# Optimization experiments

Measured on AMD Instinct MI355X. Metric: run time of the kernel, lower is better.

The kernel has to match this reference:

```python
import jax, jax.numpy as jnp
import numpy as np

B, H, W = 4, 496, 496
M = 8  # max vertices of a quad-quad convex intersection


def _corners(boxes):
    # boxes [..., 7] = (x, y, z, dx, dy, dz, heading) -> CCW BEV corners [..., 4, 2]
    x, y, dx, dy, r = boxes[..., 0], boxes[..., 1], boxes[..., 3], boxes[..., 4], boxes[..., 6]
    lx = jnp.array([0.5, -0.5, -0.5, 0.5], dtype=boxes.dtype) * dx[..., None]
    ly = jnp.array([0.5, 0.5, -0.5, -0.5], dtype=boxes.dtype) * dy[..., None]
    c, s = jnp.cos(r)[..., None], jnp.sin(r)[..., None]
    cx = x[..., None] + c * lx - s * ly
    cy = y[..., None] + s * lx + c * ly
    return jnp.stack([cx, cy], axis=-1)


def _clip(poly, cnt, a, b):
    # Clip padded CCW polygon (poly [M,2], cnt valid verts) by halfplane left of edge a->b.
    idx = jnp.arange(M)
    valid = idx < cnt
    nidx = jnp.where(idx + 1 >= cnt, 0, idx + 1)
    cur, nxt = poly, poly[nidx]
    ex, ey = b[0] - a[0], b[1] - a[1]
    dc = ex * (cur[:, 1] - a[1]) - ey * (cur[:, 0] - a[0])  # signed dist of cur
    dn = ex * (nxt[:, 1] - a[1]) - ey * (nxt[:, 0] - a[0])
    inc, inn = dc >= 0, dn >= 0
    keep = inc & valid                      # emit cur if inside
    crs = (inc != inn) & valid              # emit edge/line intersection if crossing
    den = dc - dn
    t = dc / jnp.where(jnp.abs(den) < 1e-9, 1.0, den)
    ip = cur + t[:, None] * (nxt - cur)
    c = keep.astype(jnp.int32) + crs.astype(jnp.int32)
    offs = jnp.cumsum(c) - c                # exclusive prefix sum -> output slots
    out = jnp.zeros_like(poly)
    out = out.at[jnp.where(keep, offs, M)].set(cur, mode='drop')
    out = out.at[jnp.where(crs, offs + keep.astype(jnp.int32), M)].set(ip, mode='drop')
    return out, jnp.sum(c)


def _inter_area(ca, cb):
    # Intersection area of two CCW quads (each [4,2]) via Sutherland-Hodgman.
    poly = jnp.zeros((M, 2), ca.dtype).at[:4].set(ca)
    cnt = jnp.int32(4)
    for i in range(4):
        poly, cnt = _clip(poly, cnt, cb[i], cb[(i + 1) % 4])
    idx = jnp.arange(M)
    valid = idx < cnt
    nidx = jnp.where(idx + 1 >= cnt, 0, idx + 1)
    nxt = poly[nidx]
    cr = poly[:, 0] * nxt[:, 1] - nxt[:, 0] * poly[:, 1]  # shoelace terms
    return 0.5 * jnp.abs(jnp.sum(jnp.where(valid, cr, 0.0)))


def _iou3d_aligned(boxes_a, boxes_b):
    # Element-wise (aligned) 3D oriented-box IoU. boxes [N,7] -> iou [N].
    inter_bev = jax.vmap(_inter_area)(_corners(boxes_a), _corners(boxes_b))
    za0, za1 = boxes_a[:, 2] - 0.5 * boxes_a[:, 5], boxes_a[:, 2] + 0.5 * boxes_a[:, 5]
    zb0, zb1 = boxes_b[:, 2] - 0.5 * boxes_b[:, 5], boxes_b[:, 2] + 0.5 * boxes_b[:, 5]
    zo = jnp.maximum(jnp.minimum(za1, zb1) - jnp.maximum(za0, zb0), 0.0)
    inter_vol = inter_bev * zo
    vol_a = boxes_a[:, 3] * boxes_a[:, 4] * boxes_a[:, 5]
    vol_b = boxes_b[:, 3] * boxes_b[:, 4] * boxes_b[:, 5]
    return inter_vol / (vol_a + vol_b - inter_vol + 1e-7)


def setup_inputs() -> dict:
    key = jax.random.key(0)
    kc, kd, kr, kn, km, kp, ki = jax.random.split(key, 7)
    center = jax.random.normal(kc, (B, H, W, 3), dtype=jnp.float32) * 2.0
    dims = jax.random.uniform(kd, (B, H, W, 3), minval=0.5, maxval=3.0, dtype=jnp.float32)
    heading = jax.random.uniform(kr, (B, H, W, 1), minval=-np.pi, maxval=np.pi, dtype=jnp.float32)
    box_gt = jnp.concatenate([center, dims, heading], axis=-1)  # [B,H,W,7]
    pred = box_gt + jax.random.normal(kn, box_gt.shape, dtype=jnp.float32) * 0.1
    pred = pred.at[..., 3:6].set(jnp.maximum(pred[..., 3:6], 0.2))  # keep dims positive
    box_pred = jnp.transpose(pred, (0, 3, 1, 2))  # [B,7,H,W]
    mask = jax.random.randint(km, (B, H, W), 0, 2, dtype=jnp.int32)
    iou_pred = jax.random.normal(kp, (B, H, W), dtype=jnp.float32) * 0.5
    ind = jax.random.randint(ki, (B, 128), 0, H * W, dtype=jnp.int32)  # unused by the layer
    return {"iou_pred": iou_pred, "mask": mask, "ind": ind, "box_pred": box_pred, "box_gt": box_gt}


def reference(iou_pred, mask, ind, box_pred, box_gt):
    pred = jnp.transpose(box_pred, (0, 2, 3, 1)).reshape(-1, 7)  # [N,7]
    gt = box_gt.reshape(-1, 7)
    target = 2.0 * _iou3d_aligned(pred, gt) - 1.0               # [N]
    m = mask.astype(jnp.float32).reshape(-1)
    loss = jnp.sum(m * jnp.abs(iou_pred.reshape(-1) - target))
    return loss / (jnp.sum(m) + 1e-4)
```

## Files before the change

### kernel.cpp

```cpp
#include <hip/hip_runtime.h>
#include <math.h>

#define B_   4
#define H_   496
#define W_   496
#define HW_  (H_ * W_)
#define N_   (B_ * HW_)
#define NBLK (N_ / 256)

static_assert(N_ % 256 == 0, "no tail");

__device__ __forceinline__ float clip_sum(const float px[4], const float py[4],
                                          const float qx[4], const float qy[4]) {
    float ex[4], ey[4];
#pragma unroll
    for (int i = 0; i < 4; ++i) {
        ex[i] = qx[(i + 1) & 3] - qx[i];
        ey[i] = qy[(i + 1) & 3] - qy[i];
    }
    float F[4][4];
#pragma unroll
    for (int i = 0; i < 4; ++i)
#pragma unroll
        for (int k = 0; k < 4; ++k)
            F[i][k] = ex[i] * (py[k] - qy[i]) - ey[i] * (px[k] - qx[i]);

    float s = 0.f;
#pragma unroll
    for (int k = 0; k < 4; ++k) {
        const int   k1 = (k + 1) & 3;
        const float ax = px[k], ay = py[k];
        const float dx = px[k1] - ax, dy = py[k1] - ay;
        float t0 = 0.f, t1 = 1.f;
#pragma unroll
        for (int i = 0; i < 4; ++i) {
            const float fa = F[i][k], fb = F[i][k1];
            const float df = fb - fa;
            const float dfs = (df == 0.f) ? 1e-30f : df;
            const float tc = __fdividef(-fa, dfs);
            t0 = fmaxf(t0, (df > 0.f) ? tc : 0.f);
            t1 = fminf(t1, (df < 0.f) ? tc : 1.f);
            if (df == 0.f && fa < 0.f) t0 = 2.f;
        }
        const float x0 = ax + t0 * dx, y0 = ay + t0 * dy;
        const float x1 = ax + t1 * dx, y1 = ay + t1 * dy;
        const float c  = x0 * y1 - x1 * y0;
        s += (t1 > t0) ? c : 0.f;
    }
    return s;
}

__global__ __launch_bounds__(256) void iou_main(
    const float* __restrict__ iou_pred,
    const int*   __restrict__ mask,
    const float* __restrict__ box_pred,
    const float* __restrict__ box_gt,
    float* __restrict__ ws)
{
    __shared__ float rn[4], rd[4];
    const int tid = threadIdx.x;
    const int n = blockIdx.x * 256 + tid;

    const int b  = n / HW_;
    const int hw = n - b * HW_;

    const float* bp = box_pred + (size_t)b * 7 * HW_ + hw;
    const float pax = bp[0];
    const float pay = bp[1 * HW_];
    const float paz = bp[2 * HW_];
    const float pdx = bp[3 * HW_];
    const float pdy = bp[4 * HW_];
    const float pdz = bp[5 * HW_];
    const float pr  = bp[6 * HW_];

    const float* bg = box_gt + (size_t)n * 7;
    const float gax = bg[0], gay = bg[1], gaz = bg[2];
    const float gdx = bg[3], gdy = bg[4], gdz = bg[5], gr = bg[6];

    float sp, cp; __sincosf(pr, &sp, &cp);
    float sg, cg; __sincosf(gr, &sg, &cg);
    const float phx = 0.5f * pdx, phy = 0.5f * pdy;
    const float ghx = 0.5f * gdx, ghy = 0.5f * gdy;

    float px[4], py[4], qx[4], qy[4];
    px[0] = pax + cp * phx - sp * phy;  py[0] = pay + sp * phx + cp * phy;
    px[1] = pax - cp * phx - sp * phy;  py[1] = pay - sp * phx + cp * phy;
    px[2] = pax - cp * phx + sp * phy;  py[2] = pay - sp * phx - cp * phy;
    px[3] = pax + cp * phx + sp * phy;  py[3] = pay + sp * phx - cp * phy;
    qx[0] = gax + cg * ghx - sg * ghy;  qy[0] = gay + sg * ghx + cg * ghy;
    qx[1] = gax - cg * ghx - sg * ghy;  qy[1] = gay - sg * ghx + cg * ghy;
    qx[2] = gax - cg * ghx + sg * ghy;  qy[2] = gay - sg * ghx - cg * ghy;
    qx[3] = gax + cg * ghx + sg * ghy;  qy[3] = gay + sg * ghx - cg * ghy;

    const float inter_bev = 0.5f * (clip_sum(px, py, qx, qy) +
                                    clip_sum(qx, qy, px, py));

    const float za0 = paz - 0.5f * pdz, za1 = paz + 0.5f * pdz;
    const float zb0 = gaz - 0.5f * gdz, zb1 = gaz + 0.5f * gdz;
    const float zo  = fmaxf(fminf(za1, zb1) - fmaxf(za0, zb0), 0.f);
    const float iv  = inter_bev * zo;
    const float va  = pdx * pdy * pdz;
    const float vb  = gdx * gdy * gdz;
    const float iou = iv / (va + vb - iv + 1e-7f);
    const float target = 2.f * iou - 1.f;

    const float m = (float)mask[n];
    float num = m * fabsf(iou_pred[n] - target);
    float den = m;

#pragma unroll
    for (int off = 32; off > 0; off >>= 1) {
        num += __shfl_down(num, off);
        den += __shfl_down(den, off);
    }
    if ((tid & 63) == 0) { rn[tid >> 6] = num; rd[tid >> 6] = den; }
    __syncthreads();
    if (tid == 0) {
        ws[blockIdx.x]        = rn[0] + rn[1] + rn[2] + rn[3];
        ws[NBLK + blockIdx.x] = rd[0] + rd[1] + rd[2] + rd[3];
    }
}

__global__ __launch_bounds__(256) void iou_fin(const float* __restrict__ ws,
                                               float* __restrict__ out) {
    __shared__ float rn[4], rd[4];
    float sn = 0.f, sd = 0.f;
    for (int i = threadIdx.x; i < NBLK; i += 256) {
        sn += ws[i];
        sd += ws[NBLK + i];
    }
#pragma unroll
    for (int off = 32; off > 0; off >>= 1) {
        sn += __shfl_down(sn, off);
        sd += __shfl_down(sd, off);
    }
    const int tid = threadIdx.x;
    if ((tid & 63) == 0) { rn[tid >> 6] = sn; rd[tid >> 6] = sd; }
    __syncthreads();
    if (tid == 0)
        out[0] = (rn[0] + rn[1] + rn[2] + rn[3]) /
                 (rd[0] + rd[1] + rd[2] + rd[3] + 1e-4f);
}

extern "C" void kernel_launch(void* const* d_in, const int* in_sizes, int n_in,
                              void* d_out, int out_size, void* d_ws, size_t ws_size,
                              hipStream_t stream) {
    const float* iou_pred = (const float*)d_in[0];
    const int*   mask     = (const int*)  d_in[1];
    const float* box_pred = (const float*)d_in[3];
    const float* box_gt   = (const float*)d_in[4];
    float* out = (float*)d_out;
    float* ws  = (float*)d_ws;

    iou_main<<<NBLK, 256, 0, stream>>>(iou_pred, mask, box_pred, box_gt, ws);
    iou_fin<<<1, 256, 0, stream>>>(ws, out);
}
```

Measured before the change: 121.8 us.

## Stage box_gt through LDS, process two elements per thread, simplify clip math

Each block now loads its AoS box_gt slice into shared memory with coalesced float4 loads instead of strided 7-float per-thread loads. Each thread handles two elements, which halves the block count and the partial sums. The clipping math uses FMAs, a raw reciprocal and fmed3 clamping in place of the guarded division and the degenerate-edge special case. Partials are stored as float2. The dropped df==0 handling and the use of rcp could change results on edge cases, and the larger LDS footprint may reduce occupancy.

New measurement: 108.4 us. -11.0%, faster.

```diff
diff --git a/kernel.cpp b/kernel.cpp
--- a/kernel.cpp
+++ b/kernel.cpp
@@ -6,24 +6,28 @@
 #define W_   496
 #define HW_  (H_ * W_)
 #define N_   (B_ * HW_)
-#define NBLK (N_ / 256)
+#define TPB  256
+#define NPT  2
+#define EPB  (TPB * NPT)
+#define NBLK (N_ / EPB)
 
-static_assert(N_ % 256 == 0, "no tail");
+static_assert(N_ % EPB == 0, "no tail");
 
 __device__ __forceinline__ float clip_sum(const float px[4], const float py[4],
                                           const float qx[4], const float qy[4]) {
-    float ex[4], ey[4];
+    float ex[4], ey[4], c0[4];
 #pragma unroll
     for (int i = 0; i < 4; ++i) {
         ex[i] = qx[(i + 1) & 3] - qx[i];
         ey[i] = qy[(i + 1) & 3] - qy[i];
+        c0[i] = ex[i] * qy[i] - ey[i] * qx[i];
     }
     float F[4][4];
 #pragma unroll
     for (int i = 0; i < 4; ++i)
 #pragma unroll
         for (int k = 0; k < 4; ++k)
-            F[i][k] = ex[i] * (py[k] - qy[i]) - ey[i] * (px[k] - qx[i]);
+            F[i][k] = fmaf(ex[i], py[k], fmaf(-ey[i], px[k], -c0[i]));
 
     float s = 0.f;
 #pragma unroll
@@ -36,31 +40,24 @@
         for (int i = 0; i < 4; ++i) {
             const float fa = F[i][k], fb = F[i][k1];
             const float df = fb - fa;
-            const float dfs = (df == 0.f) ? 1e-30f : df;
-            const float tc = __fdividef(-fa, dfs);
-            t0 = fmaxf(t0, (df > 0.f) ? tc : 0.f);
-            t1 = fminf(t1, (df < 0.f) ? tc : 1.f);
-            if (df == 0.f && fa < 0.f) t0 = 2.f;
+            const float tc = -fa * __builtin_amdgcn_rcpf(df);
+            const float tl = __builtin_amdgcn_fmed3f(tc, 0.f, 1.f);
+            t0 = fmaxf(t0, (df > 0.f) ? tl : 0.f);
+            t1 = fminf(t1, (df < 0.f) ? tl : 1.f);
         }
-        const float x0 = ax + t0 * dx, y0 = ay + t0 * dy;
-        const float x1 = ax + t1 * dx, y1 = ay + t1 * dy;
-        const float c  = x0 * y1 - x1 * y0;
+        const float x0 = fmaf(t0, dx, ax), y0 = fmaf(t0, dy, ay);
+        const float x1 = fmaf(t1, dx, ax), y1 = fmaf(t1, dy, ay);
+        const float c  = fmaf(x0, y1, -x1 * y0);
         s += (t1 > t0) ? c : 0.f;
     }
     return s;
 }
 
-__global__ __launch_bounds__(256) void iou_main(
-    const float* __restrict__ iou_pred,
-    const int*   __restrict__ mask,
-    const float* __restrict__ box_pred,
-    const float* __restrict__ box_gt,
-    float* __restrict__ ws)
+__device__ __forceinline__ void iou_elem(
+    int n, const float* __restrict__ iou_pred, const int* __restrict__ mask,
+    const float* __restrict__ box_pred, const float* __restrict__ sg7,
+    float& num, float& den)
 {
-    __shared__ float rn[4], rd[4];
-    const int tid = threadIdx.x;
-    const int n = blockIdx.x * 256 + tid;
-
     const int b  = n / HW_;
     const int hw = n - b * HW_;
 
@@ -73,9 +70,8 @@
     const float pdz = bp[5 * HW_];
     const float pr  = bp[6 * HW_];
 
-    const float* bg = box_gt + (size_t)n * 7;
-    const float gax = bg[0], gay = bg[1], gaz = bg[2];
-    const float gdx = bg[3], gdy = bg[4], gdz = bg[5], gr = bg[6];
+    const float gax = sg7[0], gay = sg7[1], gaz = sg7[2];
+    const float gdx = sg7[3], gdy = sg7[4], gdz = sg7[5], gr = sg7[6];
 
     float sp, cp; __sincosf(pr, &sp, &cp);
     float sg, cg; __sincosf(gr, &sg, &cg);
@@ -105,8 +101,40 @@
     const float target = 2.f * iou - 1.f;
 
     const float m = (float)mask[n];
-    float num = m * fabsf(iou_pred[n] - target);
-    float den = m;
+    num += m * fabsf(iou_pred[n] - target);
+    den += m;
+}
+
+__global__ __launch_bounds__(TPB) void iou_main(
+    const float* __restrict__ iou_pred,
+    const int*   __restrict__ mask,
+    const float* __restrict__ box_pred,
+    const float* __restrict__ box_gt,
+    float2* __restrict__ ws)
+{
+    __shared__ float sgt[EPB * 7];
+    __shared__ float rn[4], rd[4];
+
+    const int tid  = threadIdx.x;
+    const int base = blockIdx.x * EPB;
+
+    {
+        const float4* g4 = (const float4*)(box_gt + (size_t)base * 7);
+        float4* s4 = (float4*)sgt;
+#pragma unroll
+        for (int it = 0; it < (EPB * 7) / (4 * TPB); ++it)
+            s4[tid + it * TPB] = g4[tid + it * TPB];
+        const int idx = tid + 3 * TPB;
+        if (idx < (EPB * 7) / 4) s4[idx] = g4[idx];
+    }
+    __syncthreads();
+
+    float num = 0.f, den = 0.f;
+#pragma unroll
+    for (int e = 0; e < NPT; ++e) {
+        const int n = base + e * TPB + tid;
+        iou_elem(n, iou_pred, mask, box_pred, sgt + (e * TPB + tid) * 7, num, den);
+    }
 
 #pragma unroll
     for (int off = 32; off > 0; off >>= 1) {
@@ -115,19 +143,19 @@
     }
     if ((tid & 63) == 0) { rn[tid >> 6] = num; rd[tid >> 6] = den; }
     __syncthreads();
-    if (tid == 0) {
-        ws[blockIdx.x]        = rn[0] + rn[1] + rn[2] + rn[3];
-        ws[NBLK + blockIdx.x] = rd[0] + rd[1] + rd[2] + rd[3];
-    }
+    if (tid == 0)
+        ws[blockIdx.x] = make_float2(rn[0] + rn[1] + rn[2] + rn[3],
+                                     rd[0] + rd[1] + rd[2] + rd[3]);
 }
 
-__global__ __launch_bounds__(256) void iou_fin(const float* __restrict__ ws,
+__global__ __launch_bounds__(TPB) void iou_fin(const float2* __restrict__ ws,
                                                float* __restrict__ out) {
     __shared__ float rn[4], rd[4];
     float sn = 0.f, sd = 0.f;
-    for (int i = threadIdx.x; i < NBLK; i += 256) {
-        sn += ws[i];
-        sd += ws[NBLK + i];
+    for (int i = threadIdx.x; i < NBLK; i += TPB) {
+        const float2 v = ws[i];
+        sn += v.x;
+        sd += v.y;
     }
 #pragma unroll
     for (int off = 32; off > 0; off >>= 1) {
@@ -149,9 +177,9 @@
     const int*   mask     = (const int*)  d_in[1];
     const float* box_pred = (const float*)d_in[3];
     const float* box_gt   = (const float*)d_in[4];
-    float* out = (float*)d_out;
-    float* ws  = (float*)d_ws;
+    float*  out = (float*)d_out;
+    float2* ws  = (float2*)d_ws;
 
-    iou_main<<<NBLK, 256, 0, stream>>>(iou_pred, mask, box_pred, box_gt, ws);
-    iou_fin<<<1, 256, 0, stream>>>(ws, out);
+    iou_main<<<NBLK, TPB, 0, stream>>>(iou_pred, mask, box_pred, box_gt, ws);
+    iou_fin<<<1, TPB, 0, stream>>>(ws, out);
 }
```
